# Kernel tuning notes

Measured on AMD Instinct MI355X. Metric: run time of the kernel, lower is better.

Reference implementation:

```python
import jax, jax.numpy as jnp
import numpy as np

IN_CHANNELS = 512
OUT_CHANNELS = 1024
IN_CH_FACTOR = 2      # lcm(512,1024)//512
OUT_CH_FACTOR = 1     # lcm(512,1024)//1024
NUM_STEPS = 3
NUM_POINTS = 17
BATCH = 32768


def setup_inputs() -> dict:
    key = jax.random.key(0)
    k1, k2, k3, k4, k5, k6 = jax.random.split(key, 6)
    data = jax.random.normal(k1, (BATCH, IN_CHANNELS), dtype=jnp.float32)
    angles = 2.0 * jnp.pi * jax.random.uniform(k2, (NUM_POINTS,), dtype=jnp.float32)
    velocity = jax.random.uniform(k3, (NUM_POINTS,), dtype=jnp.float32)
    attention = jax.random.uniform(k4, (1, OUT_CH_FACTOR, OUT_CHANNELS, 1, 1), dtype=jnp.float32)
    coeff = 2.0 * jax.random.uniform(k5, (1,), dtype=jnp.float32) - 1.0
    bias = 2.0 * jax.random.uniform(k6, (1,), dtype=jnp.float32) - 1.0
    return {"data": data, "angles": angles, "velocity": velocity,
            "attention": attention, "coeff": coeff, "bias": bias}


def _step(d, angles, velocity, coeff, bias):
    # piecewise-linear interpolated trig activation
    index = 1.0 + jnp.tanh(d * coeff + bias) / 2.0 * NUM_POINTS
    bgn = jnp.floor(index).astype(jnp.int32)
    end = jnp.floor(index + 1.0).astype(jnp.int32)
    lt = end < NUM_POINTS
    bgn = jnp.where(lt, bgn, bgn - 1)
    end = jnp.where(lt, end, end - 1)
    pos = index - bgn.astype(index.dtype)
    # torch negative indexing wraps; replicate explicitly
    bgn_w = jnp.where(bgn < 0, bgn + NUM_POINTS, bgn)
    end_w = jnp.where(end < 0, end + NUM_POINTS, end)
    velo = (1.0 - pos) * velocity[bgn_w] + pos * velocity[end_w]
    ang = (1.0 - pos) * angles[bgn_w] + pos * angles[end_w]
    return velo * jnp.cos(ang) + d * velo * jnp.sin(ang)


def reference(data, angles, velocity, attention, coeff, bias):
    B = data.shape[0]
    # expand: [B, in_ch, 1, 1, 1] broadcast to [B, in_ch, icf, 1, 1]
    x = jnp.broadcast_to(data.reshape(B, IN_CHANNELS, 1, 1, 1),
                         (B, IN_CHANNELS, IN_CH_FACTOR, 1, 1))
    for _ in range(NUM_STEPS):
        x = x + _step(x, angles, velocity, coeff, bias) / NUM_STEPS
    # reshape to [B, ocf, out_ch, osf, out_spatio] and attention-weighted sum
    x = x.reshape(B, OUT_CH_FACTOR, OUT_CHANNELS, 1, 1)
    return jnp.sum(attention * x, axis=(1, 3))  # [B, out_ch, 1]
```

## Files before the change

### kernel.cpp

```cpp
#include <hip/hip_runtime.h>
#include <math.h>

#define BATCH        32768
#define IN_CH        512
#define OUT_CH       1024
#define NP           17
#define NSTEP        3


__global__ __launch_bounds__(256) void mac_kernel(
    const float* __restrict__ data,
    const float* __restrict__ angles,
    const float* __restrict__ velocity,
    const float* __restrict__ attention,
    const float* __restrict__ coeffp,
    const float* __restrict__ biasp,
    float* __restrict__ out)
{
    __shared__ float2 tab[NP];
    const int tid = threadIdx.x;
    if (tid < NP) {
        tab[tid] = make_float2(velocity[tid], angles[tid]);
    }
    const float coeff = coeffp[0];
    const float bias  = biasp[0];
    __syncthreads();

    const int gid = blockIdx.x * 256 + tid;
    const float4 d4 = ((const float4*)data)[gid];
    float x[4] = {d4.x, d4.y, d4.z, d4.w};

    const float HALF_NP = 8.5f;
    const float INV3    = 0.33333333333333333f;
    const float TWO     = 2.0f;

    #pragma unroll
    for (int s = 0; s < NSTEP; ++s) {
        #pragma unroll
        for (int k = 0; k < 4; ++k) {
            float dv = x[k];
            float t = fmaf(dv, coeff, bias);
            t = fminf(fmaxf(t, -15.0f), 15.0f);
            float u  = __expf(TWO * t);
            float th = (u - 1.0f) * __builtin_amdgcn_rcpf(u + 1.0f);
            float index = fmaf(th, HALF_NP, 1.0f);

            float fb = floorf(index);
            int   bgn = (int)fb;
            float fe  = floorf(index + 1.0f);
            int   end = (int)fe;
            int ib = bgn + ((bgn >> 31) & NP);
            int ie = end + ((end >> 31) & NP);

            float pos = index - fb;
            float om  = 1.0f - pos;

            float2 tb = tab[ib];
            float2 te = tab[ie];
            float velo = fmaf(om, tb.x, pos * te.x);
            float ang  = fmaf(om, tb.y, pos * te.y);

            float sn = __sinf(ang);
            float cs = __cosf(ang);
            float stp = velo * fmaf(dv, sn, cs);
            x[k] = fmaf(stp, INV3, x[k]);
        }
    }

    const int b  = gid >> 7;
    const int c4 = gid & 127;
    const float4* attv = (const float4*)attention;
    const float4 a0 = attv[c4 * 2];
    const float4 a1 = attv[c4 * 2 + 1];

    float4 o0 = make_float4(a0.x * x[0], a0.y * x[0], a0.z * x[1], a0.w * x[1]);
    float4 o1 = make_float4(a1.x * x[2], a1.y * x[2], a1.z * x[3], a1.w * x[3]);

    float4* outv = (float4*)out;
    const int base = b * 256 + c4 * 2;
    outv[base]     = o0;
    outv[base + 1] = o1;
}

extern "C" void kernel_launch(void* const* d_in, const int* in_sizes, int n_in,
                              void* d_out, int out_size, void* d_ws, size_t ws_size,
                              hipStream_t stream) {
    const float* data      = (const float*)d_in[0];
    const float* angles    = (const float*)d_in[1];
    const float* velocity  = (const float*)d_in[2];
    const float* attention = (const float*)d_in[3];
    const float* coeff     = (const float*)d_in[4];
    const float* bias      = (const float*)d_in[5];
    float* out = (float*)d_out;

    const int total_f4 = BATCH * IN_CH / 4;
    const int block = 256;
    const int grid  = total_f4 / block;
    mac_kernel<<<grid, block, 0, stream>>>(data, angles, velocity, attention,
                                           coeff, bias, out);
}
```

Measured before the change: 192.0 us.

## Precompute table deltas, simplify tanh index math, use nontemporal loads/stores

The lookup table now stores each entry's value together with the delta to the next entry, so the common path needs one shared-memory read and one FMA per interpolated quantity. The slow two-read path is kept only behind a rarely taken branch for the edge case where floor(index+1) is not floor(index)+1. The tanh-to-index computation is folded algebraically into a single reciprocal-based FMA and the clamp is dropped. Global loads and stores become nontemporal to bypass cache retention on streamed data. Because the kernel is memory-bound (about 200 MB moved), the compute savings may be hidden, and dropping the clamp relies on exp overflow behaving correctly.

Measured after the change: 192.5 us. Within noise of the previous version (+0.3%).

```diff
diff --git a/kernel.cpp b/kernel.cpp
--- a/kernel.cpp
+++ b/kernel.cpp
@@ -3,9 +3,10 @@
 
 #define BATCH        32768
 #define IN_CH        512
-#define OUT_CH       1024
 #define NP           17
 #define NSTEP        3
+
+typedef float fvec4 __attribute__((ext_vector_type(4)));
 
 
 __global__ __launch_bounds__(256) void mac_kernel(
@@ -17,22 +18,23 @@
     const float* __restrict__ biasp,
     float* __restrict__ out)
 {
-    __shared__ float2 tab[NP];
+    __shared__ fvec4 tab[NP];
     const int tid = threadIdx.x;
     if (tid < NP) {
-        tab[tid] = make_float2(velocity[tid], angles[tid]);
+        int jn = tid + 1; if (jn == NP) jn = 0;
+        float v0 = velocity[tid], a0 = angles[tid];
+        fvec4 e; e.x = v0; e.y = a0; e.z = velocity[jn] - v0; e.w = angles[jn] - a0;
+        tab[tid] = e;
     }
     const float coeff = coeffp[0];
     const float bias  = biasp[0];
     __syncthreads();
 
     const int gid = blockIdx.x * 256 + tid;
-    const float4 d4 = ((const float4*)data)[gid];
+    const fvec4 d4 = __builtin_nontemporal_load((const fvec4*)data + gid);
     float x[4] = {d4.x, d4.y, d4.z, d4.w};
 
-    const float HALF_NP = 8.5f;
-    const float INV3    = 0.33333333333333333f;
-    const float TWO     = 2.0f;
+    const float INV3 = 0.33333333333333333f;
 
     #pragma unroll
     for (int s = 0; s < NSTEP; ++s) {
@@ -40,25 +42,27 @@
         for (int k = 0; k < 4; ++k) {
             float dv = x[k];
             float t = fmaf(dv, coeff, bias);
-            t = fminf(fmaxf(t, -15.0f), 15.0f);
-            float u  = __expf(TWO * t);
-            float th = (u - 1.0f) * __builtin_amdgcn_rcpf(u + 1.0f);
-            float index = fmaf(th, HALF_NP, 1.0f);
+            float u = __expf(t + t);
+            float index = fmaf(-17.0f, __builtin_amdgcn_rcpf(u + 1.0f), 9.5f);
 
-            float fb = floorf(index);
+            float fb  = floorf(index);
             int   bgn = (int)fb;
-            float fe  = floorf(index + 1.0f);
-            int   end = (int)fe;
-            int ib = bgn + ((bgn >> 31) & NP);
-            int ie = end + ((end >> 31) & NP);
+            int   ib  = bgn + ((bgn >> 31) & NP);
+            float pos = index - fb;
 
-            float pos = index - fb;
-            float om  = 1.0f - pos;
+            fvec4 tb   = tab[ib];
+            float velo = fmaf(pos, tb.z, tb.x);
+            float ang  = fmaf(pos, tb.w, tb.y);
 
-            float2 tb = tab[ib];
-            float2 te = tab[ie];
-            float velo = fmaf(om, tb.x, pos * te.x);
-            float ang  = fmaf(om, tb.y, pos * te.y);
+            float fe = floorf(index + 1.0f);
+            if (__builtin_expect(fe != fb + 1.0f, 0)) {
+                int end = (int)fe;
+                int ie  = end + ((end >> 31) & NP);
+                fvec4 te  = tab[ie];
+                float om  = 1.0f - pos;
+                velo = fmaf(om, tb.x, pos * te.x);
+                ang  = fmaf(om, tb.y, pos * te.y);
+            }
 
             float sn = __sinf(ang);
             float cs = __cosf(ang);
@@ -69,17 +73,17 @@
 
     const int b  = gid >> 7;
     const int c4 = gid & 127;
-    const float4* attv = (const float4*)attention;
-    const float4 a0 = attv[c4 * 2];
-    const float4 a1 = attv[c4 * 2 + 1];
+    const fvec4* attv = (const fvec4*)attention;
+    const fvec4 a0 = attv[c4 * 2];
+    const fvec4 a1 = attv[c4 * 2 + 1];
 
-    float4 o0 = make_float4(a0.x * x[0], a0.y * x[0], a0.z * x[1], a0.w * x[1]);
-    float4 o1 = make_float4(a1.x * x[2], a1.y * x[2], a1.z * x[3], a1.w * x[3]);
+    fvec4 o0; o0.x = a0.x * x[0]; o0.y = a0.y * x[0]; o0.z = a0.z * x[1]; o0.w = a0.w * x[1];
+    fvec4 o1; o1.x = a1.x * x[2]; o1.y = a1.y * x[2]; o1.z = a1.z * x[3]; o1.w = a1.w * x[3];
 
-    float4* outv = (float4*)out;
+    fvec4* outv = (fvec4*)out;
     const int base = b * 256 + c4 * 2;
-    outv[base]     = o0;
-    outv[base + 1] = o1;
+    __builtin_nontemporal_store(o0, outv + base);
+    __builtin_nontemporal_store(o1, outv + base + 1);
 }
 
 extern "C" void kernel_launch(void* const* d_in, const int* in_sizes, int n_in,
```
